# Kernel optimization log

Measured on AMD Instinct MI355X. Metric: run time of the kernel, lower is better.

## Reference

```python
import jax, jax.numpy as jnp
import numpy as np
from jax import lax

N, K, FEAT, HID = 50000, 16, 64, 128


def _linear(x, w, b=None):
    y = x @ w.T
    return y + b if b is not None else y


def _lstm_aggr(dense, wih, whh, bih, bhh):
    # dense: [N, K, F]; torch-style LSTM, return hidden state at last timestep
    n = dense.shape[0]
    hdim = whh.shape[1]
    h0 = jnp.zeros((n, hdim), dense.dtype)

    def step(carry, xt):
        h, c = carry
        gates = xt @ wih.T + bih + h @ whh.T + bhh
        i, f, g, o = jnp.split(gates, 4, axis=-1)
        c = jax.nn.sigmoid(f) * c + jax.nn.sigmoid(i) * jnp.tanh(g)
        h = jax.nn.sigmoid(o) * jnp.tanh(c)
        return (h, c), None

    (h, _), _ = lax.scan(step, (h0, h0), jnp.swapaxes(dense, 0, 1))
    return h


def _sage(x, src, dst, max_deg, pw, pb, wih, whh, bih, bhh, llw, llb, lrw):
    # PyG SAGEConv(aggr='lstm', project=True): project+relu source feats,
    # gather messages, pad per-dst neighbor sequences, LSTM-aggregate,
    # then lin_l(aggr) + lin_r(x_root). dst must be sorted (it is, by construction).
    n = x.shape[0]
    xp = jax.nn.relu(_linear(x, pw, pb))
    msgs = xp[src]                                      # [E, F]
    e = src.shape[0]
    counts = jax.ops.segment_sum(jnp.ones((e,), jnp.int32), dst, num_segments=n)
    offsets = jnp.concatenate([jnp.zeros((1,), jnp.int32), jnp.cumsum(counts)[:-1]])
    pos = jnp.arange(e, dtype=jnp.int32) - offsets[dst]  # slot within neighborhood
    dense = jnp.zeros((n, max_deg, xp.shape[1]), xp.dtype).at[dst, pos].set(msgs)
    aggr = _lstm_aggr(dense, wih, whh, bih, bhh)
    return _linear(aggr, llw, llb) + _linear(x, lrw)


def setup_inputs() -> dict:
    key = jax.random.key(0)
    ks = jax.random.split(key, 16)
    s = 0.05
    dst = jnp.repeat(jnp.arange(N, dtype=jnp.int32), K)  # sorted by destination, fixed degree K
    src = jax.random.randint(ks[0], (N * K,), 0, N, dtype=jnp.int32)
    return {
        "x": jax.random.normal(ks[1], (N, FEAT), jnp.float32),
        "edge_index": jnp.stack([src, dst]),
        "max_deg": K,
        "p1_proj_w": jax.random.normal(ks[2], (FEAT, FEAT)) * s,
        "p1_proj_b": jnp.zeros((FEAT,)),
        "p1_wih": jax.random.normal(ks[3], (4 * FEAT, FEAT)) * s,
        "p1_whh": jax.random.normal(ks[4], (4 * FEAT, FEAT)) * s,
        "p1_bih": jnp.zeros((4 * FEAT,)),
        "p1_bhh": jnp.zeros((4 * FEAT,)),
        "p1_ll_w": jax.random.normal(ks[5], (HID // 2, FEAT)) * s,
        "p1_ll_b": jnp.zeros((HID // 2,)),
        "p1_lr_w": jax.random.normal(ks[6], (HID // 2, FEAT)) * s,
        "p2_proj_w": jax.random.normal(ks[7], (HID // 2, HID // 2)) * s,
        "p2_proj_b": jnp.zeros((HID // 2,)),
        "p2_wih": jax.random.normal(ks[8], (4 * (HID // 2), HID // 2)) * s,
        "p2_whh": jax.random.normal(ks[9], (4 * (HID // 2), HID // 2)) * s,
        "p2_bih": jnp.zeros((4 * (HID // 2),)),
        "p2_bhh": jnp.zeros((4 * (HID // 2),)),
        "p2_ll_w": jax.random.normal(ks[10], (HID, HID // 2)) * s,
        "p2_ll_b": jnp.zeros((HID,)),
        "p2_lr_w": jax.random.normal(ks[11], (HID, HID // 2)) * s,
        "lin1_w": jax.random.normal(ks[12], (HID * 3 // 2, HID)) * s,
        "lin1_b": jnp.zeros((HID * 3 // 2,)),
        "lin2_w": jax.random.normal(ks[13], (HID // 2, HID * 3 // 2)) * s,
        "lin2_b": jnp.zeros((HID // 2,)),
        "lin3_w": jax.random.normal(ks[14], (HID // 2, HID // 2)) * s,
        "lin3_b": jnp.zeros((HID // 2,)),
    }


def reference(x, edge_index, max_deg,
              p1_proj_w, p1_proj_b, p1_wih, p1_whh, p1_bih, p1_bhh, p1_ll_w, p1_ll_b, p1_lr_w,
              p2_proj_w, p2_proj_b, p2_wih, p2_whh, p2_bih, p2_bhh, p2_ll_w, p2_ll_b, p2_lr_w,
              lin1_w, lin1_b, lin2_w, lin2_b, lin3_w, lin3_b):
    src, dst = edge_index[0], edge_index[1]
    h = jax.nn.relu(_sage(x, src, dst, max_deg, p1_proj_w, p1_proj_b, p1_wih, p1_whh, p1_bih, p1_bhh, p1_ll_w, p1_ll_b, p1_lr_w))
    h = jax.nn.relu(_sage(h, src, dst, max_deg, p2_proj_w, p2_proj_b, p2_wih, p2_whh, p2_bih, p2_bhh, p2_ll_w, p2_ll_b, p2_lr_w))
    h = jax.nn.relu(_linear(h, lin1_w, lin1_b))
    h = jax.nn.relu(_linear(h, lin2_w, lin2_b))
    h = jax.nn.relu(_linear(h, lin3_w, lin3_b))
    return (h, edge_index)
```

## Files before the change

### kernel.cpp

```cpp
#include <hip/hip_runtime.h>
#include <hip/hip_bf16.h>

typedef unsigned short u16;
typedef unsigned int u32;
typedef __attribute__((ext_vector_type(8))) short short8;
typedef __attribute__((ext_vector_type(4))) float f32x4;

#define KS1 1.44269504f
#define KS2 2.88539008f

__device__ __forceinline__ float bf2f(u16 u) {
    union { u32 i; float f; } v; v.i = ((u32)u) << 16; return v.f;
}
__device__ __forceinline__ u16 f2bf(float f) {
    union { float f; u32 i; } v; v.f = f;
    u32 r = v.i + 0x7fffu + ((v.i >> 16) & 1u);
    return (u16)(r >> 16);
}
__device__ __forceinline__ u32 pack_bf2(float lo, float hi) {
    return __builtin_amdgcn_perm(__float_as_uint(hi), __float_as_uint(lo), 0x07060302u);
}
__device__ __forceinline__ u32 pack_relu(float a, float b) {
    return (u32)f2bf(fmaxf(a, 0.f)) | ((u32)f2bf(fmaxf(b, 0.f)) << 16);
}
__device__ __forceinline__ f32x4 bias4(const u16* b) {
    uint2 u = *(const uint2*)b;
    f32x4 r;
    r[0] = bf2f((u16)(u.x & 0xffffu)); r[1] = bf2f((u16)(u.x >> 16));
    r[2] = bf2f((u16)(u.y & 0xffffu)); r[3] = bf2f((u16)(u.y >> 16));
    return r;
}
__device__ __forceinline__ void xwrite(u16* buf, int D2, int row, int quad, int jt, u32 w0, u32 w1) {
    int ch = jt * 2 + (quad >> 1);
    *(uint2*)(buf + row * D2 + ((ch ^ (row & 7)) << 3) + ((quad & 1) << 2)) = (uint2){w0, w1};
}
__device__ __forceinline__ short8 xread(const u16* buf, int D2, int row, int quad, int kc) {
    return *(const short8*)(buf + row * D2 + (((kc * 4 + quad) ^ (row & 7)) << 3));
}
#define MFMA16 __builtin_amdgcn_mfma_f32_16x16x32_bf16

__global__ __launch_bounds__(256) void k_pre(
    const u16* __restrict__ X, const u16* __restrict__ pw, const u16* __restrict__ pb,
    u16* __restrict__ XP, int M, int gb,
    const int* __restrict__ e, float* __restrict__ eout, int n4, int eb,
    const u16* __restrict__ w1i, const u16* __restrict__ w1h,
    const u16* __restrict__ w2i, const u16* __restrict__ w2h,
    u16* __restrict__ wss)
{
    const int bid = blockIdx.x;
    const int tid = threadIdx.x;
    if (bid >= gb + eb) {
        int mi = bid - gb - eb;
        const u16* Wsrc = (mi == 0) ? w1i : (mi == 1) ? w1h : (mi == 2) ? w2i : w2h;
        u16* Wdst = wss + (size_t)mi * 16384;
        for (int idx = tid; idx < 16384; idx += 256) {
            int row = idx >> 6;
            float sc = (row >= 128 && row < 192) ? KS2 : KS1;
            Wdst[idx] = f2bf(bf2f(Wsrc[idx]) * sc);
        }
        return;
    }
    if (bid >= gb) {
        int i = (bid - gb) * 256 + tid;
        if (i < n4) {
            int4 v = *(const int4*)(e + (size_t)i * 4);
            float4 o;
            o.x = (float)v.x; o.y = (float)v.y; o.z = (float)v.z; o.w = (float)v.w;
            *(float4*)(eout + (size_t)i * 4) = o;
        }
        return;
    }
    const int lane = tid & 63;
    const int wave = tid >> 6;
    const int row0 = (bid * 4 + wave) * 16;
    if (row0 >= M) return;
    const int col  = lane & 15;
    const int quad = lane >> 4;

    f32x4 c1[4];
#pragma unroll
    for (int jt = 0; jt < 4; ++jt) c1[jt] = (f32x4){0.f, 0.f, 0.f, 0.f};
    {
        const u16* xrow = X  + (size_t)(row0 + col) * 64 + quad * 8;
        const u16* wrow = pw + (size_t)col * 64 + quad * 8;
#pragma unroll
        for (int kc = 0; kc < 64; kc += 32) {
            short8 a = *(const short8*)(xrow + kc);
#pragma unroll
            for (int jt = 0; jt < 4; ++jt) {
                short8 b = *(const short8*)(wrow + (size_t)jt * 16 * 64 + kc);
                c1[jt] = MFMA16(a, b, c1[jt], 0, 0, 0);
            }
        }
    }
#pragma unroll
    for (int jt = 0; jt < 4; ++jt) {
        float bias = bf2f(pb[jt * 16 + col]);
#pragma unroll
        for (int r = 0; r < 4; ++r) {
            float v = fmaxf(c1[jt][r] + bias, 0.f);
            XP[(size_t)(row0 + quad * 4 + r) * 64 + jt * 16 + col] = f2bf(v);
        }
    }
}


#define NONLIN(ACC, CST, HW0, HW1)                                             \
    {                                                                          \
        float hv[4];                                                           \
        _Pragma("unroll") for (int r = 0; r < 4; ++r) {                        \
            float iv = ACC[0][r], fv = ACC[1][r], gv = ACC[2][r], ov = ACC[3][r]; \
            float e_i = __builtin_amdgcn_exp2f(-iv);                           \
            float e_f = __builtin_amdgcn_exp2f(-fv);                           \
            float e_g = __builtin_amdgcn_exp2f(gv);                            \
            float af  = 1.0f + e_f;                                            \
            float P   = (1.0f + e_i) * (1.0f + e_g);                           \
            float tt  = __builtin_fmaf(e_g, KS2, -KS2);                        \
            float num = __builtin_fmaf(tt, af, CST[r] * P);                    \
            float cn  = num * __builtin_amdgcn_rcpf(af * P);                   \
            CST[r] = cn;                                                       \
            float e_c = __builtin_amdgcn_exp2f(cn);                            \
            float e_o = __builtin_amdgcn_exp2f(-ov);                           \
            float roc = __builtin_amdgcn_rcpf((1.0f + e_o) * (1.0f + e_c));    \
            hv[r] = (e_c - 1.0f) * roc;                                        \
        }                                                                      \
        HW0 = pack_bf2(hv[0], hv[1]);                                          \
        HW1 = pack_bf2(hv[2], hv[3]);                                          \
    }

#define LSTMS_PROLOGUE                                                         \
    const int tid  = threadIdx.x;                                              \
    const int lane = tid & 63;                                                 \
    const int w    = tid >> 6;                                                 \
    const int col  = lane & 15;                                                \
    const int quad = lane >> 4;                                                \
    const int node0 = blockIdx.x * 16;                                         \
    if (node0 >= N) return;                                                    \
    const int nodeA = node0 + col;                                             \
    const bool act  = nodeA < N;                                               \
    const int ndA   = act ? nodeA : (N - 1);                                   \
    {                                                                          \
        int j = tid;                                                           \
        float sc = (j >= 128 && j < 192) ? KS2 : KS1;                          \
        lds_b[j] = (bf2f(bih[j]) + bf2f(bhh[j])) * sc;                         \
    }                                                                          \
    {                                                                          \
        const int rr   = lane >> 3;                  \
        const int ch   = lane & 7;                   \
        const int slot = ch ^ rr;                    \
        _Pragma("unroll") for (int half = 0; half < 2; ++half) {               \
            int sik[4];                                                        \
            _Pragma("unroll") for (int k = 0; k < 4; ++k) {                    \
                int kk = half * 4 + k;                                         \
                int t  = w * 4 + (kk >> 1);                                    \
                int r  = (kk & 1) * 8 + rr;                                    \
                int nrow = node0 + r; if (nrow >= N) nrow = N - 1;             \
                sik[k] = src[nrow * 16 + t];                                   \
            }                                                                  \
            short8 vk[4];                                                      \
            _Pragma("unroll") for (int k = 0; k < 4; ++k)                      \
                vk[k] = *(const short8*)(xp + (size_t)sik[k] * 64 + ch * 8);   \
            _Pragma("unroll") for (int k = 0; k < 4; ++k) {                    \
                int kk = half * 4 + k;                                         \
                int t  = w * 4 + (kk >> 1);                                    \
                int r  = (kk & 1) * 8 + rr;                                    \
                *(short8*)(xs + t * 1024 + r * 64 + slot * 8) = vk[k];         \
            }                                                                  \
        }                                                                      \
    }                                                                          \
    short8 wf[8], hf[8];                                                       \
    _Pragma("unroll") for (int g = 0; g < 4; ++g) {                            \
        int jt = w + 4 * g;                                                    \
        const u16* wi = wihs + (size_t)(jt * 16 + col) * 64 + quad * 8;        \
        const u16* wh = whhs + (size_t)(jt * 16 + col) * 64 + quad * 8;        \
        wf[g * 2 + 0] = *(const short8*)(wi);                                  \
        wf[g * 2 + 1] = *(const short8*)(wi + 32);                             \
        hf[g * 2 + 0] = *(const short8*)(wh);                                  \
        hf[g * 2 + 1] = *(const short8*)(wh + 32);                             \
    }                                                                          \
    __syncthreads();                                                           \
    const int q0 = quad ^ (col & 7);                                           \
    short8 xbA0, xbA1;                                                         \
    {                                                                          \
        const u16* p = xs + col * 64;                                          \
        xbA0 = *(const short8*)(p + q0 * 8);                                   \
        xbA1 = *(const short8*)(p + (q0 ^ 4) * 8);                             \
    }

#define LSTMS_CORE_LOOP                                                        \
    short8 hbA0 = (short8){0,0,0,0,0,0,0,0};                                   \
    short8 hbA1 = hbA0;                                                        \
    float cA[4];                                                               \
    _Pragma("unroll") for (int i = 0; i < 4; ++i) cA[i] = 0.f;                 \
    _Pragma("unroll 1") for (int t = 0; t < 16; ++t) {                         \
        u16* hbuf = lds_h[t & 1];                                              \
        f32x4 acc[4];                                                          \
        _Pragma("unroll") for (int g = 0; g < 4; ++g) {                        \
            f32x4 bc = *(const f32x4*)(lds_b + (w + 4 * g) * 16 + quad * 4);   \
            acc[g] = MFMA16(wf[g * 2 + 0], xbA0, bc, 0, 0, 0);                 \
            acc[g] = MFMA16(wf[g * 2 + 1], xbA1, acc[g], 0, 0, 0);             \
        }                                                                      \
        short8 xn0 = xbA0, xn1 = xbA1;                                         \
        if (t < 15) {                                                          \
            const u16* p = xs + (t + 1) * 1024 + col * 64;                     \
            xn0 = *(const short8*)(p + q0 * 8);                                \
            xn1 = *(const short8*)(p + (q0 ^ 4) * 8);                          \
        }                                                                      \
        if (t > 0) {                                                           \
            _Pragma("unroll") for (int g = 0; g < 4; ++g) {                    \
                acc[g] = MFMA16(hf[g * 2 + 0], hbA0, acc[g], 0, 0, 0);         \
                acc[g] = MFMA16(hf[g * 2 + 1], hbA1, acc[g], 0, 0, 0);         \
            }                                                                  \
        }                                                                      \
        u32 hwA0, hwA1;                                                        \
        NONLIN(acc, cA, hwA0, hwA1)                                            \
        xwrite(hbuf, 64, col, quad, w, hwA0, hwA1);                            \
        __syncthreads();                                                       \
        hbA0 = xread(hbuf, 64, col, quad, 0);                                  \
        hbA1 = xread(hbuf, 64, col, quad, 1);                                  \
        xbA0 = xn0; xbA1 = xn1;                                                \
    }

__global__ __launch_bounds__(256, 4) void lstm_mid(
    const u16* __restrict__ xp, const int* __restrict__ src,
    const u16* __restrict__ wihs, const u16* __restrict__ whhs,
    const u16* __restrict__ bih, const u16* __restrict__ bhh,
    const u16* __restrict__ X,
    const u16* __restrict__ llw, const u16* __restrict__ llb,
    const u16* __restrict__ lrw,
    const u16* __restrict__ pw, const u16* __restrict__ pb,
    u16* __restrict__ Y1, u16* __restrict__ XP2, int N)
{
    __shared__ u16 xs[16 * 1024];
    __shared__ float lds_b[256];
    __shared__ u16 lds_h[2][16 * 64];
    u16* bufY = xs;

    LSTMS_PROLOGUE
    LSTMS_CORE_LOOP

    {
        const u16* wr  = llw + (size_t)(w * 16 + col) * 64 + quad * 8;
        short8 ll0 = *(const short8*)wr, ll1 = *(const short8*)(wr + 32);
        const u16* wr2 = lrw + (size_t)(w * 16 + col) * 64 + quad * 8;
        short8 lr0 = *(const short8*)wr2, lr1 = *(const short8*)(wr2 + 32);
        f32x4 bY = bias4(llb + w * 16 + quad * 4);

        const u16* xrA = X + (size_t)ndA * 64 + quad * 8;
        short8 rxA0 = *(const short8*)xrA, rxA1 = *(const short8*)(xrA + 32);

        f32x4 aA = MFMA16(ll0, hbA0, bY, 0, 0, 0);
        aA = MFMA16(ll1, hbA1, aA, 0, 0, 0);
        aA = MFMA16(lr0, rxA0, aA, 0, 0, 0);
        aA = MFMA16(lr1, rxA1, aA, 0, 0, 0);

        u32 yA0 = pack_relu(aA[0], aA[1]), yA1 = pack_relu(aA[2], aA[3]);
        if (act) *(uint2*)(Y1 + (size_t)nodeA * 64 + w * 16 + quad * 4) = (uint2){yA0, yA1};
        xwrite(bufY, 64, col, quad, w, yA0, yA1);
        __syncthreads();

        const u16* wp = pw + (size_t)(w * 16 + col) * 64 + quad * 8;
        short8 p0 = *(const short8*)wp, p1 = *(const short8*)(wp + 32);
        f32x4 bp = bias4(pb + w * 16 + quad * 4);

        short8 ybA0 = xread(bufY, 64, col, quad, 0);
        short8 ybA1 = xread(bufY, 64, col, quad, 1);

        f32x4 a2A = MFMA16(p0, ybA0, bp, 0, 0, 0);
        a2A = MFMA16(p1, ybA1, a2A, 0, 0, 0);

        if (act) *(uint2*)(XP2 + (size_t)nodeA * 64 + w * 16 + quad * 4) =
            (uint2){pack_relu(a2A[0], a2A[1]), pack_relu(a2A[2], a2A[3])};
    }
}

__global__ __launch_bounds__(256, 4) void lstm_post(
    const u16* __restrict__ xp, const int* __restrict__ src,
    const u16* __restrict__ wihs, const u16* __restrict__ whhs,
    const u16* __restrict__ bih, const u16* __restrict__ bhh,
    const u16* __restrict__ Y1,
    const u16* __restrict__ llw2, const u16* __restrict__ llb2,
    const u16* __restrict__ lrw2,
    const u16* __restrict__ w1m, const u16* __restrict__ b1m,
    const u16* __restrict__ w2m, const u16* __restrict__ b2m,
    const u16* __restrict__ w3m, const u16* __restrict__ b3m,
    float* __restrict__ outp, int N)
{
    __shared__ u16 xs[16 * 1024];
    __shared__ float lds_b[256];
    __shared__ u16 lds_h[2][16 * 64];
    u16* bufA = xs;
    u16* bufB = xs + 2048;

    LSTMS_PROLOGUE
    LSTMS_CORE_LOOP

    {
        const u16* yrA = Y1 + (size_t)ndA * 64 + quad * 8;
        short8 ryA0 = *(const short8*)yrA, ryA1 = *(const short8*)(yrA + 32);

#pragma unroll
        for (int ti = 0; ti < 2; ++ti) {
            int jt = 2 * w + ti;
            const u16* wr = llw2 + (size_t)(jt * 16 + col) * 64 + quad * 8;
            short8 l0 = *(const short8*)wr, l1 = *(const short8*)(wr + 32);
            const u16* wr2 = lrw2 + (size_t)(jt * 16 + col) * 64 + quad * 8;
            short8 r0 = *(const short8*)wr2, r1 = *(const short8*)(wr2 + 32);
            f32x4 b0 = bias4(llb2 + jt * 16 + quad * 4);
            f32x4 aA = MFMA16(l0, hbA0, b0, 0, 0, 0);
            aA = MFMA16(l1, hbA1, aA, 0, 0, 0);
            aA = MFMA16(r0, ryA0, aA, 0, 0, 0);
            aA = MFMA16(r1, ryA1, aA, 0, 0, 0);
            xwrite(bufA, 128, col, quad, jt, pack_relu(aA[0], aA[1]), pack_relu(aA[2], aA[3]));
        }
        __syncthreads();

        short8 y2A[4];
#pragma unroll
        for (int kc = 0; kc < 4; ++kc) y2A[kc] = xread(bufA, 128, col, quad, kc);

#pragma unroll
        for (int ti = 0; ti < 3; ++ti) {
            int jt = 3 * w + ti;
            const u16* wr = w1m + (size_t)(jt * 16 + col) * 128 + quad * 8;
            short8 wk[4];
#pragma unroll
            for (int kc = 0; kc < 4; ++kc) wk[kc] = *(const short8*)(wr + kc * 32);
            f32x4 b1v = bias4(b1m + jt * 16 + quad * 4);
            f32x4 aA = b1v;
#pragma unroll
            for (int kc = 0; kc < 4; ++kc) aA = MFMA16(wk[kc], y2A[kc], aA, 0, 0, 0);
            xwrite(bufB, 192, col, quad, jt, pack_relu(aA[0], aA[1]), pack_relu(aA[2], aA[3]));
        }
        __syncthreads();

        short8 t1A[6];
#pragma unroll
        for (int kc = 0; kc < 6; ++kc) t1A[kc] = xread(bufB, 192, col, quad, kc);

        {
            const u16* wr = w2m + (size_t)(w * 16 + col) * 192 + quad * 8;
            f32x4 b2v = bias4(b2m + w * 16 + quad * 4);
            f32x4 aA = b2v;
#pragma unroll
            for (int kc = 0; kc < 6; ++kc) {
                short8 wk = *(const short8*)(wr + kc * 32);
                aA = MFMA16(wk, t1A[kc], aA, 0, 0, 0);
            }
            xwrite(bufA, 64, col, quad, w, pack_relu(aA[0], aA[1]), pack_relu(aA[2], aA[3]));
        }
        __syncthreads();

        short8 t2A0 = xread(bufA, 64, col, quad, 0);
        short8 t2A1 = xread(bufA, 64, col, quad, 1);
        {
            const u16* wr = w3m + (size_t)(w * 16 + col) * 64 + quad * 8;
            short8 l0 = *(const short8*)wr, l1 = *(const short8*)(wr + 32);
            f32x4 b3v = bias4(b3m + w * 16 + quad * 4);
            f32x4 aA = MFMA16(l0, t2A0, b3v, 0, 0, 0);
            aA = MFMA16(l1, t2A1, aA, 0, 0, 0);
            if (act) {
                float4 oA;
                oA.x = fmaxf(aA[0], 0.f); oA.y = fmaxf(aA[1], 0.f);
                oA.z = fmaxf(aA[2], 0.f); oA.w = fmaxf(aA[3], 0.f);
                *(float4*)(outp + (size_t)nodeA * 64 + w * 16 + quad * 4) = oA;
            }
        }
    }
}

extern "C" void kernel_launch(void* const* d_in, const int* in_sizes, int n_in,
                              void* d_out, int out_size, void* d_ws, size_t ws_size,
                              hipStream_t stream)
{
    const u16* x       = (const u16*)d_in[0];
    const int* edge    = (const int*)d_in[1];
    const u16* p1_pw   = (const u16*)d_in[3];
    const u16* p1_pb   = (const u16*)d_in[4];
    const u16* p1_wih  = (const u16*)d_in[5];
    const u16* p1_whh  = (const u16*)d_in[6];
    const u16* p1_bih  = (const u16*)d_in[7];
    const u16* p1_bhh  = (const u16*)d_in[8];
    const u16* p1_llw  = (const u16*)d_in[9];
    const u16* p1_llb  = (const u16*)d_in[10];
    const u16* p1_lrw  = (const u16*)d_in[11];
    const u16* p2_pw   = (const u16*)d_in[12];
    const u16* p2_pb   = (const u16*)d_in[13];
    const u16* p2_wih  = (const u16*)d_in[14];
    const u16* p2_whh  = (const u16*)d_in[15];
    const u16* p2_bih  = (const u16*)d_in[16];
    const u16* p2_bhh  = (const u16*)d_in[17];
    const u16* p2_llw  = (const u16*)d_in[18];
    const u16* p2_llb  = (const u16*)d_in[19];
    const u16* p2_lrw  = (const u16*)d_in[20];
    const u16* lin1w   = (const u16*)d_in[21];
    const u16* lin1b   = (const u16*)d_in[22];
    const u16* lin2w   = (const u16*)d_in[23];
    const u16* lin2b   = (const u16*)d_in[24];
    const u16* lin3w   = (const u16*)d_in[25];
    const u16* lin3b   = (const u16*)d_in[26];
    (void)n_in; (void)ws_size;

    const int N  = in_sizes[0] / 64;
    const int E2 = in_sizes[1];
    const int* srcIdx = edge;

    char* w = (char*)d_ws;
    u16* wss   = (u16*)(w);
    u16* xp1   = (u16*)(w + 1u  * 1024 * 1024);
    u16* xp2   = (u16*)(w + 8u  * 1024 * 1024);
    u16* bufY1 = (u16*)(w + 15u * 1024 * 1024);
    u16* wih1s = wss;
    u16* whh1s = wss + 16384;
    u16* wih2s = wss + 32768;
    u16* whh2s = wss + 49152;

    float* out_h    = (float*)d_out;
    float* out_edge = (float*)d_out + (size_t)N * 64;
    (void)out_size;

    const int gb  = (N + 63) / 64;
    const int gbl = (N + 15) / 16;
    const int n4 = E2 / 4;
    const int eb = (n4 + 255) / 256;

    dim3 block(256);

    hipLaunchKernelGGL(k_pre, dim3(gb + eb + 4), block, 0, stream,
                       x, p1_pw, p1_pb, xp1, N, gb,
                       edge, out_edge, n4, eb,
                       p1_wih, p1_whh, p2_wih, p2_whh, wss);
    hipLaunchKernelGGL(lstm_mid, dim3(gbl), block, 0, stream,
                       xp1, srcIdx, wih1s, whh1s, p1_bih, p1_bhh,
                       x, p1_llw, p1_llb, p1_lrw, p2_pw, p2_pb, bufY1, xp2, N);
    hipLaunchKernelGGL(lstm_post, dim3(gbl), block, 0, stream,
                       xp2, srcIdx, wih2s, whh2s, p2_bih, p2_bhh,
                       bufY1, p2_llw, p2_llb, p2_lrw,
                       lin1w, lin1b, lin2w, lin2b, lin3w, lin3b, out_h, N);
}
```

Before: 279.5 us.

## Stream LSTM neighbor gathers into a half-size LDS ring with direct global-to-LDS loads

The neighbor feature gather now uses global_load_lds to copy straight into LDS. The 16 timesteps go through an 8-slot ring: the first 8 are loaded up front and the later ones are issued at steps 4 and 8, with waits on vmcnt. This halves the xs shared buffer, which lowers LDS use per block and may allow more blocks per CU, and it overlaps the gather latency with the recurrence. The per-step barrier becomes a bare s_barrier after waiting only on lgkmcnt. The weight prescale in k_pre is also spread over 64 blocks with vectorized accesses. Ordering relies on the manual waitcnt placement and ring-slot reuse, so a mistake there could produce races.

```diff
diff --git a/kernel.cpp b/kernel.cpp
--- a/kernel.cpp
+++ b/kernel.cpp
@@ -29,6 +29,15 @@
     r[0] = bf2f((u16)(u.x & 0xffffu)); r[1] = bf2f((u16)(u.x >> 16));
     r[2] = bf2f((u16)(u.y & 0xffffu)); r[3] = bf2f((u16)(u.y >> 16));
     return r;
+}
+__device__ __forceinline__ void barrier_lds() {
+    asm volatile("s_waitcnt lgkmcnt(0)" ::: "memory");
+    __builtin_amdgcn_s_barrier();
+}
+__device__ __forceinline__ void gload_lds16(const u16* g, u16* l) {
+    __builtin_amdgcn_global_load_lds(
+        (const __attribute__((address_space(1))) u32*)(const void*)g,
+        (__attribute__((address_space(3))) u32*)(void*)l, 16, 0, 0);
 }
 __device__ __forceinline__ void xwrite(u16* buf, int D2, int row, int quad, int jt, u32 w0, u32 w1) {
     int ch = jt * 2 + (quad >> 1);
@@ -50,14 +59,19 @@
     const int bid = blockIdx.x;
     const int tid = threadIdx.x;
     if (bid >= gb + eb) {
-        int mi = bid - gb - eb;
+        int wb = bid - gb - eb;
+        int mi = wb >> 4;
         const u16* Wsrc = (mi == 0) ? w1i : (mi == 1) ? w1h : (mi == 2) ? w2i : w2h;
         u16* Wdst = wss + (size_t)mi * 16384;
-        for (int idx = tid; idx < 16384; idx += 256) {
-            int row = idx >> 6;
-            float sc = (row >= 128 && row < 192) ? KS2 : KS1;
-            Wdst[idx] = f2bf(bf2f(Wsrc[idx]) * sc);
-        }
+        int e0 = (wb & 15) * 1024 + tid * 4;
+        int row = e0 >> 6;
+        float sc = (row >= 128 && row < 192) ? KS2 : KS1;
+        uint2 v = *(const uint2*)(Wsrc + e0);
+        u32 a = (u32)f2bf(bf2f((u16)(v.x & 0xffffu)) * sc)
+              | ((u32)f2bf(bf2f((u16)(v.x >> 16)) * sc) << 16);
+        u32 b = (u32)f2bf(bf2f((u16)(v.y & 0xffffu)) * sc)
+              | ((u32)f2bf(bf2f((u16)(v.y >> 16)) * sc) << 16);
+        *(uint2*)(Wdst + e0) = (uint2){a, b};
         return;
     }
     if (bid >= gb) {
@@ -144,29 +158,22 @@
         float sc = (j >= 128 && j < 192) ? KS2 : KS1;                          \
         lds_b[j] = (bf2f(bih[j]) + bf2f(bhh[j])) * sc;                         \
     }                                                                          \
+    const int rlo = lane >> 3;                               \
+    const u16* gch = xp + (((lane & 7) ^ rlo) << 3);   \
+    int i20, i21, i30, i31;                                                    \
     {                                                                          \
-        const int rr   = lane >> 3;                  \
-        const int ch   = lane & 7;                   \
-        const int slot = ch ^ rr;                    \
-        _Pragma("unroll") for (int half = 0; half < 2; ++half) {               \
-            int sik[4];                                                        \
-            _Pragma("unroll") for (int k = 0; k < 4; ++k) {                    \
-                int kk = half * 4 + k;                                         \
-                int t  = w * 4 + (kk >> 1);                                    \
-                int r  = (kk & 1) * 8 + rr;                                    \
-                int nrow = node0 + r; if (nrow >= N) nrow = N - 1;             \
-                sik[k] = src[nrow * 16 + t];                                   \
-            }                                                                  \
-            short8 vk[4];                                                      \
-            _Pragma("unroll") for (int k = 0; k < 4; ++k)                      \
-                vk[k] = *(const short8*)(xp + (size_t)sik[k] * 64 + ch * 8);   \
-            _Pragma("unroll") for (int k = 0; k < 4; ++k) {                    \
-                int kk = half * 4 + k;                                         \
-                int t  = w * 4 + (kk >> 1);                                    \
-                int r  = (kk & 1) * 8 + rr;                                    \
-                *(short8*)(xs + t * 1024 + r * 64 + slot * 8) = vk[k];         \
-            }                                                                  \
-        }                                                                      \
+        int r0n = node0 + rlo;     if (r0n >= N) r0n = N - 1;                  \
+        int r1n = node0 + 8 + rlo; if (r1n >= N) r1n = N - 1;                  \
+        const int* s0 = src + (size_t)r0n * 16 + w;                            \
+        const int* s1 = src + (size_t)r1n * 16 + w;                            \
+        int i00 = s0[0],  i01 = s1[0];                  \
+        int i10 = s0[4],  i11 = s1[4];                  \
+        i20 = s0[8];  i21 = s1[8];                      \
+        i30 = s0[12]; i31 = s1[12];                     \
+        gload_lds16(gch + (size_t)i00 * 64, xs + w * 1024);                    \
+        gload_lds16(gch + (size_t)i01 * 64, xs + w * 1024 + 512);              \
+        gload_lds16(gch + (size_t)i10 * 64, xs + (4 + w) * 1024);              \
+        gload_lds16(gch + (size_t)i11 * 64, xs + (4 + w) * 1024 + 512);        \
     }                                                                          \
     short8 wf[8], hf[8];                                                       \
     _Pragma("unroll") for (int g = 0; g < 4; ++g) {                            \
@@ -184,7 +191,7 @@
     {                                                                          \
         const u16* p = xs + col * 64;                                          \
         xbA0 = *(const short8*)(p + q0 * 8);                                   \
-        xbA1 = *(const short8*)(p + (q0 ^ 4) * 8);                             \
+        xbA1 = *(const short8*)(p + ((q0 ^ 4) << 3));                          \
     }
 
 #define LSTMS_CORE_LOOP                                                        \
@@ -193,6 +200,16 @@
     float cA[4];                                                               \
     _Pragma("unroll") for (int i = 0; i < 4; ++i) cA[i] = 0.f;                 \
     _Pragma("unroll 1") for (int t = 0; t < 16; ++t) {                         \
+        if (t == 7 || t == 11)                                                 \
+            asm volatile("s_waitcnt vmcnt(0)" ::: "memory");                   \
+        if (t == 4) {            \
+            gload_lds16(gch + (size_t)i20 * 64, xs + w * 1024);                \
+            gload_lds16(gch + (size_t)i21 * 64, xs + w * 1024 + 512);          \
+        }                                                                      \
+        if (t == 8) {           \
+            gload_lds16(gch + (size_t)i30 * 64, xs + (4 + w) * 1024);          \
+            gload_lds16(gch + (size_t)i31 * 64, xs + (4 + w) * 1024 + 512);    \
+        }                                                                      \
         u16* hbuf = lds_h[t & 1];                                              \
         f32x4 acc[4];                                                          \
         _Pragma("unroll") for (int g = 0; g < 4; ++g) {                        \
@@ -202,9 +219,11 @@
         }                                                                      \
         short8 xn0 = xbA0, xn1 = xbA1;                                         \
         if (t < 15) {                                                          \
-            const u16* p = xs + (t + 1) * 1024 + col * 64;                     \
+            int s = t + 1;                                                     \
+            const u16* p = xs + ((((s >> 2) & 1) * 4 + (s & 3)) * 1024)        \
+                              + col * 64;                                      \
             xn0 = *(const short8*)(p + q0 * 8);                                \
-            xn1 = *(const short8*)(p + (q0 ^ 4) * 8);                          \
+            xn1 = *(const short8*)(p + ((q0 ^ 4) << 3));                       \
         }                                                                      \
         if (t > 0) {                                                           \
             _Pragma("unroll") for (int g = 0; g < 4; ++g) {                    \
@@ -215,7 +234,7 @@
         u32 hwA0, hwA1;                                                        \
         NONLIN(acc, cA, hwA0, hwA1)                                            \
         xwrite(hbuf, 64, col, quad, w, hwA0, hwA1);                            \
-        __syncthreads();                                                       \
+        barrier_lds();                                                         \
         hbA0 = xread(hbuf, 64, col, quad, 0);                                  \
         hbA1 = xread(hbuf, 64, col, quad, 1);                                  \
         xbA0 = xn0; xbA1 = xn1;                                                \
@@ -231,7 +250,7 @@
     const u16* __restrict__ pw, const u16* __restrict__ pb,
     u16* __restrict__ Y1, u16* __restrict__ XP2, int N)
 {
-    __shared__ u16 xs[16 * 1024];
+    __shared__ u16 xs[8 * 1024];
     __shared__ float lds_b[256];
     __shared__ u16 lds_h[2][16 * 64];
     u16* bufY = xs;
@@ -286,7 +305,7 @@
     const u16* __restrict__ w3m, const u16* __restrict__ b3m,
     float* __restrict__ outp, int N)
 {
-    __shared__ u16 xs[16 * 1024];
+    __shared__ u16 xs[8 * 1024];
     __shared__ float lds_b[256];
     __shared__ u16 lds_h[2][16 * 64];
     u16* bufA = xs;
@@ -426,7 +445,7 @@
 
     dim3 block(256);
 
-    hipLaunchKernelGGL(k_pre, dim3(gb + eb + 4), block, 0, stream,
+    hipLaunchKernelGGL(k_pre, dim3(gb + eb + 64), block, 0, stream,
                        x, p1_pw, p1_pb, xp1, N, gb,
                        edge, out_edge, n4, eb,
                        p1_wih, p1_whh, p2_wih, p2_whh, wss);
```

Measured after the change: 286.7 us. +2.6%, slower.
